# Kernel optimization log

Hardware: AMD Instinct MI355X
Metric: run time of the kernel (lower is better)

The kernel has to match this reference:

```python
import jax, jax.numpy as jnp
import numpy as np

K = 1024
D = 256
BETA = 0.25


def setup_inputs() -> dict:
    key = jax.random.key(0)
    k1, k2 = jax.random.split(key)
    inputs = jax.random.normal(k1, (16, D, 4096), dtype=jnp.float32)  # (B, D, T)
    # embedding.weight.data.uniform_(-1/K, 1/K)
    weight = jax.random.uniform(k2, (K, D), dtype=jnp.float32, minval=-1.0 / K, maxval=1.0 / K)
    return {"inputs": inputs, "weight": weight}


def reference(inputs, weight):
    B, Dd, T = inputs.shape
    x = jnp.transpose(inputs, (0, 2, 1))          # (B, T, D)
    flat = x.reshape(-1, Dd)                      # (N, D), N = B*T
    in_sqr = jnp.sum(flat * flat, axis=1, keepdims=True)     # (N, 1)
    embed_sqr = jnp.sum(weight * weight, axis=1)             # (K,)
    dis = in_sqr + embed_sqr - 2.0 * (flat @ weight.T)       # (N, K)
    ind = jnp.argmin(dis, axis=1)                            # (N,)
    quant = weight[ind].reshape(B, T, Dd)                    # gather == one-hot @ weight
    vq = jnp.mean((jax.lax.stop_gradient(quant) - x) ** 2)
    commit = jnp.mean((quant - jax.lax.stop_gradient(x)) ** 2)
    vq_loss = BETA * vq + commit
    quant_st = x + jax.lax.stop_gradient(quant - x)          # straight-through
    N = flat.shape[0]
    counts = jnp.zeros((K,), dtype=jnp.float32).at[ind].add(1.0)
    avg_probs = counts / N
    perp = jnp.exp(-jnp.sum(avg_probs * jnp.log(avg_probs + 1e-10)))
    return jnp.transpose(quant_st, (0, 2, 1)), vq_loss, perp
```

## Files before the change

### kernel.cpp

```cpp
#include <hip/hip_runtime.h>
#include <hip/hip_bf16.h>


#define DD   256
#define KK   1024
#define TT   4096
#define BBB  16
#define NROW (BBB*TT)

typedef _Float16 half8 __attribute__((ext_vector_type(8)));
typedef float f32x4 __attribute__((ext_vector_type(4)));

__device__ __forceinline__ unsigned umaxu(unsigned a, unsigned b) { return a > b ? a : b; }
__device__ __forceinline__ unsigned uminu(unsigned a, unsigned b) { return a < b ? a : b; }

__global__ void prep(const float* __restrict__ w, _Float16* __restrict__ w16,
                     unsigned* __restrict__ counts, double* __restrict__ lsum,
                     float* __restrict__ wsq) {
    int gid = blockIdx.x * 256 + threadIdx.x;
    int k = gid >> 5;
    int c = gid & 31;
    int chunk = k >> 4, n = k & 15;
    int ks = c >> 2, q = c & 3;
    const float* src = w + (k << 8) + (c << 3);
    union { uint4 u; _Float16 h[8]; } pk;
#pragma unroll
    for (int j = 0; j < 8; ++j) pk.h[j] = (_Float16)(src[j] * 1024.0f);
    size_t dst = ((((size_t)chunk * 8 + ks) * 4 + q) * 16 + n) * 8;
    *(uint4*)(w16 + dst) = pk.u;
    if (c == 0) {
        const float4* wr4 = (const float4*)(w + (k << 8));
        float s = 0.f;
#pragma unroll 8
        for (int ii = 0; ii < 64; ++ii) {
            float4 v = wr4[ii];
            s += v.x * v.x + v.y * v.y + v.z * v.z + v.w * v.w;
        }
        wsq[k] = 512.0f * s;
    }
    if (gid < KK) counts[gid] = 0u;
    if (gid == KK) *lsum = 0.0;
}


#define LOADB(PFX, chn) do {                                                   \
    const uint4* _p = wsrc + ((chn) << 9) + lane;                              \
    PFX##0 = *(const half8*)(_p);                                              \
    PFX##1 = *(const half8*)(_p + 64);                                         \
    PFX##2 = *(const half8*)(_p + 128);                                        \
    PFX##3 = *(const half8*)(_p + 192);                                        \
    PFX##4 = *(const half8*)(_p + 256);                                        \
    PFX##5 = *(const half8*)(_p + 320);                                        \
    PFX##6 = *(const half8*)(_p + 384);                                        \
    PFX##7 = *(const half8*)(_p + 448);                                        \
} while (0)

#define MFMA16(A, B, C) __builtin_amdgcn_mfma_f32_16x16x32_f16((A), (B), (C), 0, 0, 0)

#define COMPUTE(ch, PFX) do {                                                  \
    f32x4 a0 = {0.f, 0.f, 0.f, 0.f};                                           \
    f32x4 a1 = {0.f, 0.f, 0.f, 0.f};                                           \
    a0 = MFMA16(afrag[0][0], PFX##0, a0); a1 = MFMA16(afrag[1][0], PFX##0, a1);\
    a0 = MFMA16(afrag[0][1], PFX##1, a0); a1 = MFMA16(afrag[1][1], PFX##1, a1);\
    a0 = MFMA16(afrag[0][2], PFX##2, a0); a1 = MFMA16(afrag[1][2], PFX##2, a1);\
    a0 = MFMA16(afrag[0][3], PFX##3, a0); a1 = MFMA16(afrag[1][3], PFX##3, a1);\
    a0 = MFMA16(afrag[0][4], PFX##4, a0); a1 = MFMA16(afrag[1][4], PFX##4, a1);\
    a0 = MFMA16(afrag[0][5], PFX##5, a0); a1 = MFMA16(afrag[1][5], PFX##5, a1);\
    a0 = MFMA16(afrag[0][6], PFX##6, a0); a1 = MFMA16(afrag[1][6], PFX##6, a1);\
    a0 = MFMA16(afrag[0][7], PFX##7, a0); a1 = MFMA16(afrag[1][7], PFX##7, a1);\
    unsigned kg = (unsigned)(((ch) << 4) + n);                                 \
    float csub = wsql[kg];                                                     \
    _Pragma("unroll")                                                          \
    for (int i = 0; i < 4; ++i) {                                              \
        float v; unsigned p, o;                                                \
        v = fmaxf(a0[i] - csub, 0.0f);                                         \
        p = (__float_as_uint(v) & 0xFFFFFC00u) | kg;                           \
        o = b1[i];                                                             \
        b2[i] = umaxu(b2[i], uminu(p, o));                                     \
        b1[i] = umaxu(o, p);                                                   \
        v = fmaxf(a1[i] - csub, 0.0f);                                         \
        p = (__float_as_uint(v) & 0xFFFFFC00u) | kg;                           \
        o = b1[4 + i];                                                         \
        b2[4 + i] = umaxu(b2[4 + i], uminu(p, o));                             \
        b1[4 + i] = umaxu(o, p);                                               \
    }                                                                          \
} while (0)

__global__ __launch_bounds__(256, 2) void stageA(const float* __restrict__ x,
                                                 const _Float16* __restrict__ w16,
                                                 const float* __restrict__ wsq,
                                                 uint4* __restrict__ cand) {
    __shared__ __align__(16) float wsql[KK];
    int tid = threadIdx.x, bid = blockIdx.x;
    int b = bid >> 5;
    int t0 = (bid & 31) << 7;
    const float* xbase = x + ((size_t)b << 20) + t0;

    int lane = tid & 63, wv = tid >> 6;
    int n = lane & 15, q = lane >> 4;

    ((float4*)wsql)[tid] = ((const float4*)wsq)[tid];

    half8 afrag[2][8];
#pragma unroll
    for (int mt = 0; mt < 2; ++mt) {
        int rl = (wv << 5) + (mt << 4) + n;
#pragma unroll
        for (int ks = 0; ks < 8; ++ks) {
            const float* p = xbase + (((size_t)((ks << 5) + (q << 3))) << 12) + rl;
            half8 f;
#pragma unroll
            for (int j = 0; j < 8; ++j) f[j] = (_Float16)p[(size_t)j << 12];
            afrag[mt][ks] = f;
        }
    }
    __syncthreads();

    unsigned b1[8], b2[8];
#pragma unroll
    for (int i = 0; i < 8; ++i) { b1[i] = 0u; b2[i] = 0u; }

    const uint4* wsrc = (const uint4*)w16;

    half8 bA0, bA1, bA2, bA3, bA4, bA5, bA6, bA7;
    half8 bB0, bB1, bB2, bB3, bB4, bB5, bB6, bB7;

    LOADB(bA, 0);
    for (int ch = 0; ch < 64; ch += 2) {
        LOADB(bB, ch + 1);
        COMPUTE(ch, bA);
        if (ch + 2 < 64) LOADB(bA, ch + 2);
        COMPUTE(ch + 1, bB);
    }

#pragma unroll
    for (int s = 0; s < 8; ++s) {
        unsigned v0 = b1[s], v1 = b2[s], v2 = 0u, v3 = 0u;
#pragma unroll
        for (int m = 1; m <= 8; m <<= 1) {
            unsigned e0 = __shfl_xor(v0, m);
            unsigned e1 = __shfl_xor(v1, m);
            unsigned e2 = __shfl_xor(v2, m);
            unsigned e3 = __shfl_xor(v3, m);
#pragma unroll
            for (int u = 0; u < 4; ++u) {
                unsigned e = (u == 0) ? e0 : (u == 1) ? e1 : (u == 2) ? e2 : e3;
                unsigned t;
                t = umaxu(e, v0); e = uminu(e, v0); v0 = t;
                t = umaxu(e, v1); e = uminu(e, v1); v1 = t;
                t = umaxu(e, v2); e = uminu(e, v2); v2 = t;
                v3 = umaxu(e, v3);
            }
        }
        if (n == 0) {
            int row_local = (wv << 5) + ((s >> 2) << 4) + (q << 2) + (s & 3);
            cand[(bid << 7) + row_local] = make_uint4(v0, v1, v2, v3);
        }
    }
}

#define XLS 257
__global__ __launch_bounds__(256) void stageBC(const float* __restrict__ x,
                                               const float* __restrict__ w,
                                               const uint4* __restrict__ cand,
                                               float* __restrict__ out,
                                               unsigned* __restrict__ counts,
                                               double* __restrict__ lsum) {
    __shared__ __align__(16) float xl[32 * XLS];
    __shared__ double disl[32][4];
    __shared__ int winner[32];
    __shared__ double ldis[32];
    int tid = threadIdx.x, bid = blockIdx.x;
    int b = bid >> 7, t0 = (bid & 127) << 5;
    int lane = tid & 63, wv = tid >> 6;

    {
        int dr = tid >> 3;
        int t4 = (tid & 7) << 2;
        const float* xb = x + ((size_t)b << 20) + t0 + t4;
#pragma unroll
        for (int pass = 0; pass < 8; ++pass) {
            int d = (pass << 5) + dr;
            float4 v = *(const float4*)(xb + ((size_t)d << 12));
            xl[(t4 + 0) * XLS + d] = v.x;
            xl[(t4 + 1) * XLS + d] = v.y;
            xl[(t4 + 2) * XLS + d] = v.z;
            xl[(t4 + 3) * XLS + d] = v.w;
        }
    }
    __syncthreads();

    int c = lane >> 4, dl = lane & 15;
#pragma unroll
    for (int rr = 0; rr < 8; ++rr) {
        int r = (wv << 3) + rr;
        int rowg = (b << 12) + t0 + r;
        unsigned ci = ((const unsigned*)cand)[((size_t)rowg << 2) + c] & 1023u;
        const float* wr = w + (ci << 8);
        double s = 0.0;
#pragma unroll
        for (int dd = 0; dd < 4; ++dd) {
            int d4 = (dd << 6) + (dl << 2);
            float4 xv = *(const float4*)(&xl[r * XLS + d4]);
            float4 wv4 = *(const float4*)(wr + d4);
            double e;
            e = (double)xv.x - (double)wv4.x; s = fma(e, e, s);
            e = (double)xv.y - (double)wv4.y; s = fma(e, e, s);
            e = (double)xv.z - (double)wv4.z; s = fma(e, e, s);
            e = (double)xv.w - (double)wv4.w; s = fma(e, e, s);
        }
#pragma unroll
        for (int m = 1; m <= 8; m <<= 1) s += __shfl_xor(s, m);
        if (dl == 0) disl[r][c] = s;
    }
    __syncthreads();

    if (tid < 32) {
        int rowg = (b << 12) + t0 + tid;
        uint4 cc = cand[rowg];
        unsigned i0 = cc.x & 1023u, i1 = cc.y & 1023u, i2 = cc.z & 1023u, i3 = cc.w & 1023u;
        double dm = disl[tid][0]; unsigned ci = i0;
        double dk;
        dk = disl[tid][1]; if (dk < dm || (dk == dm && i1 < ci)) { dm = dk; ci = i1; }
        dk = disl[tid][2]; if (dk < dm || (dk == dm && i2 < ci)) { dm = dk; ci = i2; }
        dk = disl[tid][3]; if (dk < dm || (dk == dm && i3 < ci)) { dm = dk; ci = i3; }
        winner[tid] = (int)ci;
        ldis[tid] = dm;
        atomicAdd(&counts[ci], 1u);
    }
    __syncthreads();

    float* wg = xl;
#pragma unroll
    for (int rp = 0; rp < 8; ++rp) {
        int r = (rp << 2) + wv;
        int win = winner[r];
        *(float4*)(&wg[r * XLS + (lane << 2)]) =
            *(const float4*)(w + (win << 8) + (lane << 2));
    }
    __syncthreads();

    {
        int dr = tid >> 3;
        int t4 = (tid & 7) << 2;
        float* ob = out + ((size_t)b << 20) + t0 + t4;
#pragma unroll
        for (int pass = 0; pass < 8; ++pass) {
            int d = (pass << 5) + dr;
            float4 o;
            o.x = wg[(t4 + 0) * XLS + d];
            o.y = wg[(t4 + 1) * XLS + d];
            o.z = wg[(t4 + 2) * XLS + d];
            o.w = wg[(t4 + 3) * XLS + d];
            *(float4*)(ob + ((size_t)d << 12)) = o;
        }
    }

    __syncthreads();
    if (tid < 16) ldis[tid] += ldis[tid + 16];
    __syncthreads();
    if (tid < 8) ldis[tid] += ldis[tid + 8];
    __syncthreads();
    if (tid < 4) ldis[tid] += ldis[tid + 4];
    __syncthreads();
    if (tid < 2) ldis[tid] += ldis[tid + 2];
    __syncthreads();
    if (tid == 0) atomicAdd(lsum, ldis[0] + ldis[1]);
}

__global__ void finalize(const unsigned* __restrict__ counts,
                         const double* __restrict__ lsum,
                         float* __restrict__ out2) {
    __shared__ double part[256];
    int tid = threadIdx.x;
    double s = 0.0;
    for (int i = tid; i < KK; i += 256) {
        double p = (double)counts[i] / (double)NROW;
        s += p * log(p + 1e-10);
    }
    part[tid] = s;
    __syncthreads();
    for (int st = 128; st > 0; st >>= 1) {
        if (tid < st) part[tid] += part[tid + st];
        __syncthreads();
    }
    if (tid == 0) {
        out2[0] = (float)(1.25 * (*lsum) / ((double)NROW * (double)DD));
        out2[1] = (float)exp(-part[0]);
    }
}

extern "C" void kernel_launch(void* const* d_in, const int* in_sizes, int n_in,
                              void* d_out, int out_size, void* d_ws, size_t ws_size,
                              hipStream_t stream) {
    const float* x = (const float*)d_in[0];
    const float* w = (const float*)d_in[1];
    float* out = (float*)d_out;
    char* ws = (char*)d_ws;
    _Float16* w16    = (_Float16*)ws;
    uint4*    cnd    = (uint4*)(ws + 524288);
    unsigned* counts = (unsigned*)(ws + 1572864);
    float*    wsq    = (float*)(ws + 1576960);
    double*   lsum   = (double*)(ws + 1581056);

    prep<<<128, 256, 0, stream>>>(w, w16, counts, lsum, wsq);
    stageA<<<512, 256, 0, stream>>>(x, w16, wsq, (uint4*)cnd);
    stageBC<<<2048, 256, 0, stream>>>(x, w, (const uint4*)cnd, out, counts, lsum);
    finalize<<<1, 256, 0, stream>>>(counts, lsum, out + (size_t)NROW * DD);
}
```

Measured before the change: 196.4 us.

## Fuse candidate search and exact rescoring into one kernel via shared-memory x tiles

Merges stageA (fp16 MFMA top-4 candidate search) and stageBC (fp64 rescoring, gather and output write) into a single kernel. Each 128-row block stages x through a padded LDS tile in four 32-row pieces, and the candidates stay in shared memory instead of a global buffer. This removes the candidate round-trip through global memory and one kernel launch. The price is that x is read from global memory twice within the block (once for the A fragments, once for rescoring), many serial __syncthreads phases run in each block, and only 512 blocks handle the BC work instead of 2048, which lowers parallelism and LDS-limited occupancy for that phase.

```diff
diff --git a/kernel.cpp b/kernel.cpp
--- a/kernel.cpp
+++ b/kernel.cpp
@@ -42,6 +42,22 @@
     if (gid == KK) *lsum = 0.0;
 }
 
+#define XLS 257
+
+#define XLOAD(toff) do {                                                       \
+    int _dr = tid >> 3;                                                        \
+    int _t4 = (tid & 7) << 2;                                                  \
+    const float* _xb = x + ((size_t)b << 20) + t0 + (toff) + _t4;              \
+    _Pragma("unroll")                                                          \
+    for (int _pass = 0; _pass < 8; ++_pass) {                                  \
+        int _d = (_pass << 5) + _dr;                                           \
+        float4 _v = *(const float4*)(_xb + ((size_t)_d << 12));                \
+        xt[(_t4 + 0) * XLS + _d] = _v.x;                                       \
+        xt[(_t4 + 1) * XLS + _d] = _v.y;                                       \
+        xt[(_t4 + 2) * XLS + _d] = _v.z;                                       \
+        xt[(_t4 + 3) * XLS + _d] = _v.w;                                       \
+    }                                                                          \
+} while (0)
 
 #define LOADB(PFX, chn) do {                                                   \
     const uint4* _p = wsrc + ((chn) << 9) + lane;                              \
@@ -86,16 +102,23 @@
     }                                                                          \
 } while (0)
 
-__global__ __launch_bounds__(256, 2) void stageA(const float* __restrict__ x,
-                                                 const _Float16* __restrict__ w16,
-                                                 const float* __restrict__ wsq,
-                                                 uint4* __restrict__ cand) {
+__global__ __launch_bounds__(256, 2) void fused(const float* __restrict__ x,
+                                                const float* __restrict__ w,
+                                                const _Float16* __restrict__ w16,
+                                                const float* __restrict__ wsq,
+                                                float* __restrict__ out,
+                                                unsigned* __restrict__ counts,
+                                                double* __restrict__ lsum) {
+    __shared__ __align__(16) float xt[32 * XLS];
     __shared__ __align__(16) float wsql[KK];
+    __shared__ __align__(16) uint4 cndl[128];
+    __shared__ double disl[32][4];
+    __shared__ int winner[32];
+    __shared__ double ldis[32];
+
     int tid = threadIdx.x, bid = blockIdx.x;
     int b = bid >> 5;
     int t0 = (bid & 31) << 7;
-    const float* xbase = x + ((size_t)b << 20) + t0;
-
     int lane = tid & 63, wv = tid >> 6;
     int n = lane & 15, q = lane >> 4;
 
@@ -103,25 +126,31 @@
 
     half8 afrag[2][8];
 #pragma unroll
-    for (int mt = 0; mt < 2; ++mt) {
-        int rl = (wv << 5) + (mt << 4) + n;
-#pragma unroll
-        for (int ks = 0; ks < 8; ++ks) {
-            const float* p = xbase + (((size_t)((ks << 5) + (q << 3))) << 12) + rl;
-            half8 f;
-#pragma unroll
-            for (int j = 0; j < 8; ++j) f[j] = (_Float16)p[(size_t)j << 12];
-            afrag[mt][ks] = f;
-        }
-    }
-    __syncthreads();
+    for (int p = 0; p < 4; ++p) {
+        XLOAD(p << 5);
+        __syncthreads();
+        if (wv == p) {
+#pragma unroll
+            for (int mt = 0; mt < 2; ++mt) {
+                int rl = (mt << 4) + n;
+#pragma unroll
+                for (int ks = 0; ks < 8; ++ks) {
+                    const float* sp = &xt[rl * XLS + (ks << 5) + (q << 3)];
+                    half8 f;
+#pragma unroll
+                    for (int j = 0; j < 8; ++j) f[j] = (_Float16)sp[j];
+                    afrag[mt][ks] = f;
+                }
+            }
+        }
+        __syncthreads();
+    }
 
     unsigned b1[8], b2[8];
 #pragma unroll
     for (int i = 0; i < 8; ++i) { b1[i] = 0u; b2[i] = 0u; }
 
     const uint4* wsrc = (const uint4*)w16;
-
     half8 bA0, bA1, bA2, bA3, bA4, bA5, bA6, bA7;
     half8 bB0, bB1, bB2, bB3, bB4, bB5, bB6, bB7;
 
@@ -154,118 +183,90 @@
         }
         if (n == 0) {
             int row_local = (wv << 5) + ((s >> 2) << 4) + (q << 2) + (s & 3);
-            cand[(bid << 7) + row_local] = make_uint4(v0, v1, v2, v3);
-        }
-    }
-}
-
-#define XLS 257
-__global__ __launch_bounds__(256) void stageBC(const float* __restrict__ x,
-                                               const float* __restrict__ w,
-                                               const uint4* __restrict__ cand,
-                                               float* __restrict__ out,
-                                               unsigned* __restrict__ counts,
-                                               double* __restrict__ lsum) {
-    __shared__ __align__(16) float xl[32 * XLS];
-    __shared__ double disl[32][4];
-    __shared__ int winner[32];
-    __shared__ double ldis[32];
-    int tid = threadIdx.x, bid = blockIdx.x;
-    int b = bid >> 7, t0 = (bid & 127) << 5;
-    int lane = tid & 63, wv = tid >> 6;
-
-    {
-        int dr = tid >> 3;
-        int t4 = (tid & 7) << 2;
-        const float* xb = x + ((size_t)b << 20) + t0 + t4;
-#pragma unroll
-        for (int pass = 0; pass < 8; ++pass) {
-            int d = (pass << 5) + dr;
-            float4 v = *(const float4*)(xb + ((size_t)d << 12));
-            xl[(t4 + 0) * XLS + d] = v.x;
-            xl[(t4 + 1) * XLS + d] = v.y;
-            xl[(t4 + 2) * XLS + d] = v.z;
-            xl[(t4 + 3) * XLS + d] = v.w;
+            cndl[row_local] = make_uint4(v0, v1, v2, v3);
         }
     }
     __syncthreads();
 
     int c = lane >> 4, dl = lane & 15;
-#pragma unroll
-    for (int rr = 0; rr < 8; ++rr) {
-        int r = (wv << 3) + rr;
-        int rowg = (b << 12) + t0 + r;
-        unsigned ci = ((const unsigned*)cand)[((size_t)rowg << 2) + c] & 1023u;
-        const float* wr = w + (ci << 8);
-        double s = 0.0;
-#pragma unroll
-        for (int dd = 0; dd < 4; ++dd) {
-            int d4 = (dd << 6) + (dl << 2);
-            float4 xv = *(const float4*)(&xl[r * XLS + d4]);
-            float4 wv4 = *(const float4*)(wr + d4);
-            double e;
-            e = (double)xv.x - (double)wv4.x; s = fma(e, e, s);
-            e = (double)xv.y - (double)wv4.y; s = fma(e, e, s);
-            e = (double)xv.z - (double)wv4.z; s = fma(e, e, s);
-            e = (double)xv.w - (double)wv4.w; s = fma(e, e, s);
-        }
-#pragma unroll
-        for (int m = 1; m <= 8; m <<= 1) s += __shfl_xor(s, m);
-        if (dl == 0) disl[r][c] = s;
-    }
-    __syncthreads();
-
-    if (tid < 32) {
-        int rowg = (b << 12) + t0 + tid;
-        uint4 cc = cand[rowg];
-        unsigned i0 = cc.x & 1023u, i1 = cc.y & 1023u, i2 = cc.z & 1023u, i3 = cc.w & 1023u;
-        double dm = disl[tid][0]; unsigned ci = i0;
-        double dk;
-        dk = disl[tid][1]; if (dk < dm || (dk == dm && i1 < ci)) { dm = dk; ci = i1; }
-        dk = disl[tid][2]; if (dk < dm || (dk == dm && i2 < ci)) { dm = dk; ci = i2; }
-        dk = disl[tid][3]; if (dk < dm || (dk == dm && i3 < ci)) { dm = dk; ci = i3; }
-        winner[tid] = (int)ci;
-        ldis[tid] = dm;
-        atomicAdd(&counts[ci], 1u);
-    }
-    __syncthreads();
-
-    float* wg = xl;
-#pragma unroll
-    for (int rp = 0; rp < 8; ++rp) {
-        int r = (rp << 2) + wv;
-        int win = winner[r];
-        *(float4*)(&wg[r * XLS + (lane << 2)]) =
-            *(const float4*)(w + (win << 8) + (lane << 2));
-    }
-    __syncthreads();
-
-    {
-        int dr = tid >> 3;
-        int t4 = (tid & 7) << 2;
-        float* ob = out + ((size_t)b << 20) + t0 + t4;
-#pragma unroll
-        for (int pass = 0; pass < 8; ++pass) {
-            int d = (pass << 5) + dr;
-            float4 o;
-            o.x = wg[(t4 + 0) * XLS + d];
-            o.y = wg[(t4 + 1) * XLS + d];
-            o.z = wg[(t4 + 2) * XLS + d];
-            o.w = wg[(t4 + 3) * XLS + d];
-            *(float4*)(ob + ((size_t)d << 12)) = o;
-        }
-    }
-
-    __syncthreads();
-    if (tid < 16) ldis[tid] += ldis[tid + 16];
-    __syncthreads();
-    if (tid < 8) ldis[tid] += ldis[tid + 8];
-    __syncthreads();
-    if (tid < 4) ldis[tid] += ldis[tid + 4];
-    __syncthreads();
-    if (tid < 2) ldis[tid] += ldis[tid + 2];
-    __syncthreads();
-    if (tid == 0) atomicAdd(lsum, ldis[0] + ldis[1]);
+    for (int qt = 0; qt < 4; ++qt) {
+        XLOAD(qt << 5);
+        __syncthreads();
+
+#pragma unroll
+        for (int rr = 0; rr < 8; ++rr) {
+            int r = (wv << 3) + rr;
+            unsigned ci = ((const unsigned*)cndl)[(((qt << 5) + r) << 2) + c] & 1023u;
+            const float* wr = w + (ci << 8);
+            double s = 0.0;
+#pragma unroll
+            for (int dd = 0; dd < 4; ++dd) {
+                int d4 = (dd << 6) + (dl << 2);
+                float4 xv = *(const float4*)(&xt[r * XLS + d4]);
+                float4 wv4 = *(const float4*)(wr + d4);
+                double e;
+                e = (double)xv.x - (double)wv4.x; s = fma(e, e, s);
+                e = (double)xv.y - (double)wv4.y; s = fma(e, e, s);
+                e = (double)xv.z - (double)wv4.z; s = fma(e, e, s);
+                e = (double)xv.w - (double)wv4.w; s = fma(e, e, s);
+            }
+#pragma unroll
+            for (int m = 1; m <= 8; m <<= 1) s += __shfl_xor(s, m);
+            if (dl == 0) disl[r][c] = s;
+        }
+        __syncthreads();
+
+        if (tid < 32) {
+            uint4 cc = cndl[(qt << 5) + tid];
+            unsigned i0 = cc.x & 1023u, i1 = cc.y & 1023u, i2 = cc.z & 1023u, i3 = cc.w & 1023u;
+            double dm = disl[tid][0]; unsigned ci = i0;
+            double dk;
+            dk = disl[tid][1]; if (dk < dm || (dk == dm && i1 < ci)) { dm = dk; ci = i1; }
+            dk = disl[tid][2]; if (dk < dm || (dk == dm && i2 < ci)) { dm = dk; ci = i2; }
+            dk = disl[tid][3]; if (dk < dm || (dk == dm && i3 < ci)) { dm = dk; ci = i3; }
+            winner[tid] = (int)ci;
+            ldis[tid] = dm;
+            atomicAdd(&counts[ci], 1u);
+        }
+        __syncthreads();
+
+#pragma unroll
+        for (int rp = 0; rp < 8; ++rp) {
+            int r = (rp << 2) + wv;
+            int win = winner[r];
+            *(float4*)(&xt[r * XLS + (lane << 2)]) =
+                *(const float4*)(w + (win << 8) + (lane << 2));
+        }
+        __syncthreads();
+
+        {
+            int dr = tid >> 3;
+            int t4 = (tid & 7) << 2;
+            float* ob = out + ((size_t)b << 20) + t0 + (qt << 5) + t4;
+#pragma unroll
+            for (int pass = 0; pass < 8; ++pass) {
+                int d = (pass << 5) + dr;
+                float4 o;
+                o.x = xt[(t4 + 0) * XLS + d];
+                o.y = xt[(t4 + 1) * XLS + d];
+                o.z = xt[(t4 + 2) * XLS + d];
+                o.w = xt[(t4 + 3) * XLS + d];
+                *(float4*)(ob + ((size_t)d << 12)) = o;
+            }
+        }
+
+        __syncthreads();
+        if (tid < 16) ldis[tid] += ldis[tid + 16];
+        __syncthreads();
+        if (tid < 8) ldis[tid] += ldis[tid + 8];
+        __syncthreads();
+        if (tid < 4) ldis[tid] += ldis[tid + 4];
+        __syncthreads();
+        if (tid < 2) ldis[tid] += ldis[tid + 2];
+        __syncthreads();
+        if (tid == 0) atomicAdd(lsum, ldis[0] + ldis[1]);
+        __syncthreads();
+    }
 }
 
 __global__ void finalize(const unsigned* __restrict__ counts,
@@ -298,13 +299,11 @@
     float* out = (float*)d_out;
     char* ws = (char*)d_ws;
     _Float16* w16    = (_Float16*)ws;
-    uint4*    cnd    = (uint4*)(ws + 524288);
-    unsigned* counts = (unsigned*)(ws + 1572864);
-    float*    wsq    = (float*)(ws + 1576960);
-    double*   lsum   = (double*)(ws + 1581056);
+    unsigned* counts = (unsigned*)(ws + 524288);
+    float*    wsq    = (float*)(ws + 528384);
+    double*   lsum   = (double*)(ws + 532480);
 
     prep<<<128, 256, 0, stream>>>(w, w16, counts, lsum, wsq);
-    stageA<<<512, 256, 0, stream>>>(x, w16, wsq, (uint4*)cnd);
-    stageBC<<<2048, 256, 0, stream>>>(x, w, (const uint4*)cnd, out, counts, lsum);
+    fused<<<512, 256, 0, stream>>>(x, w, w16, wsq, out, counts, lsum);
     finalize<<<1, 256, 0, stream>>>(counts, lsum, out + (size_t)NROW * DD);
 }
```

Measured after the change: 186.5 us. 5.0% less time.
